# Kernel optimization log

Hardware: AMD Instinct MI355X
Metric: run time of the kernel (lower is better)

## Reference

```python
import jax, jax.numpy as jnp
import numpy as np

N_NODES = 50000
N_EDGES = 800000
NUM_GRAPHS = 16
NUM_CLASSES = 247


def _glorot(key, shape):
    fan_in = shape[0]
    return jax.random.normal(key, shape, jnp.float32) * (1.0 / np.sqrt(fan_in))


def setup_inputs() -> dict:
    key = jax.random.key(0)
    ks = jax.random.split(key, 8)
    x = jax.random.normal(ks[0], (N_NODES, 3), jnp.float32)
    edge_index = jax.random.randint(ks[1], (2, N_EDGES), 0, N_NODES, dtype=jnp.int64 if jax.config.jax_enable_x64 else jnp.int32)
    batch = jnp.sort(jax.random.randint(ks[2], (N_NODES,), 0, NUM_GRAPHS))
    return {
        "x": x,
        "edge_index": edge_index,
        "batch": batch,
        "W1": _glorot(ks[3], (3, 64)),
        "b1": jnp.zeros((64,), jnp.float32),
        "W2": _glorot(ks[4], (64, 128)),
        "b2": jnp.zeros((128,), jnp.float32),
        "W3": _glorot(ks[5], (128, 256)),
        "b3": jnp.zeros((256,), jnp.float32),
        "Wfc": _glorot(ks[6], (256, NUM_CLASSES)),
        "bfc": jnp.zeros((NUM_CLASSES,), jnp.float32),
    }


def reference(x, edge_index, batch, W1, b1, W2, b2, W3, b3, Wfc, bfc):
    N = x.shape[0]
    # --- GCN symmetric normalization with self-loops (PyG gcn_norm) ---
    loops = jnp.arange(N, dtype=edge_index.dtype)
    ei = jnp.concatenate([edge_index, jnp.stack([loops, loops])], axis=1)
    row, col = ei[0], ei[1]  # src -> dst, aggregate at dst
    deg = jax.ops.segment_sum(jnp.ones(ei.shape[1], x.dtype), col, num_segments=N)
    dinv = jnp.where(deg > 0, jax.lax.rsqrt(deg), 0.0)
    norm = dinv[row] * dinv[col]  # [E+N]

    def gcn(h, W, b):
        h = h @ W                                    # [N, out]
        msg = h[row] * norm[:, None]                 # gather + scale
        agg = jax.ops.segment_sum(msg, col, num_segments=N)  # scatter-add
        return agg + b

    h = jax.nn.relu(gcn(x, W1, b1))
    h = jax.nn.relu(gcn(h, W2, b2))
    h = jax.nn.relu(gcn(h, W3, b3))

    # --- global_mean_pool over batch indices ---
    sums = jax.ops.segment_sum(h, batch, num_segments=NUM_GRAPHS)      # [G, 256]
    cnt = jax.ops.segment_sum(jnp.ones(N, h.dtype), batch, num_segments=NUM_GRAPHS)
    pooled = sums / jnp.maximum(cnt, 1.0)[:, None]

    return pooled @ Wfc + bfc  # [G, num_classes]
```

## Files before the change

### kernel.cpp

```cpp
#include <hip/hip_runtime.h>

#define N_NODES 50000
#define N_EDGES 800000
#define NUM_GRAPHS 16
#define NUM_CLASSES 247
#define SCAN_BLOCKS ((N_NODES + 255) / 256)
#define CSR_CAP (N_EDGES + 7 * N_NODES)

typedef __attribute__((ext_vector_type(8))) short bf16x8;
typedef __attribute__((ext_vector_type(4))) float f32x4;

static inline int nblk(long n) { return (int)((n + 255) / 256); }

__device__ __forceinline__ float bfl(unsigned short u) {
    return __uint_as_float((unsigned)u << 16);
}
__device__ __forceinline__ unsigned short bf16_rne(float f) {
    unsigned u = __float_as_uint(f);
    u += 0x7FFF + ((u >> 16) & 1);
    return (unsigned short)(u >> 16);
}

__device__ __forceinline__ unsigned q8(float v) {
    if (v < 0.015625f) return 0u;
    unsigned u = __float_as_uint(v) - (120u << 23);
    u += 0x3FFFF + ((u >> 19) & 1);
    unsigned q = u >> 19;
    return q > 255u ? 255u : q;
}
__device__ __forceinline__ float dq8(unsigned x) {
    float f = __uint_as_float((x + 1920u) << 19);
    return x ? f : 0.0f;
}

__global__ void k_deg(const int* __restrict__ col, int* __restrict__ degc,
                      int* __restrict__ pos, int E) {
    int e = blockIdx.x * blockDim.x + threadIdx.x;
    if (e >= E) return;
    int c8 = (e >> 8) & 7;
    pos[e] = atomicAdd(&degc[c8 * N_NODES + col[e]], 1);
}

__global__ __launch_bounds__(256) void k_scan1(const int* __restrict__ degc,
                                               int* __restrict__ rowptr,
                                               int* __restrict__ bsum,
                                               const int* __restrict__ batch,
                                               float* __restrict__ pcnt, int N) {
    __shared__ int buf[256];
    __shared__ int hist[NUM_GRAPHS];
    int t = threadIdx.x;
    if (t < NUM_GRAPHS) hist[t] = 0;
    __syncthreads();
    int i = blockIdx.x * 256 + t;
    int v = 0;
    if (i < N) {
        int tot = 0;
#pragma unroll
        for (int c = 0; c < 8; ++c) tot += degc[c * N_NODES + i];
        v = (tot + 7) & ~7;
        atomicAdd(&hist[batch[i]], 1);
    }
    buf[t] = v;
    __syncthreads();
#pragma unroll
    for (int off = 1; off < 256; off <<= 1) {
        int tmp = (t >= off) ? buf[t - off] : 0;
        __syncthreads();
        if (t >= off) buf[t] += tmp;
        __syncthreads();
    }
    if (i < N) rowptr[i] = buf[t] - v;
    if (t == 255) bsum[blockIdx.x] = buf[255];
    if (t < NUM_GRAPHS && hist[t] > 0) atomicAdd(&pcnt[t], (float)hist[t]);
}

__global__ __launch_bounds__(256) void k_scan3(int* __restrict__ rowptr,
                                               const int* __restrict__ bsum,
                                               const int* __restrict__ degc,
                                               int* __restrict__ base,
                                               float* __restrict__ dinv,
                                               const float* __restrict__ x,
                                               float* __restrict__ xs,
                                               int* __restrict__ csr,
                                               const float* __restrict__ W2,
                                               const float* __restrict__ W3,
                                               unsigned short* __restrict__ Wt2,
                                               unsigned short* __restrict__ Wt3,
                                               int N) {
    __shared__ int red[256];
    int t = threadIdx.x;
    int b = blockIdx.x;
    red[t] = (t < b) ? bsum[t] : 0;
    __syncthreads();
#pragma unroll
    for (int off = 128; off > 0; off >>= 1) {
        if (t < off) red[t] += red[t + off];
        __syncthreads();
    }
    int boff = red[0];
    int i = b * 256 + t;
    if (i < N) {
        int rp = rowptr[i] + boff;
        rowptr[i] = rp;
        int run = rp, tot = 0;
#pragma unroll
        for (int c = 0; c < 8; ++c) {
            int d = degc[c * N_NODES + i];
            base[c * N_NODES + i] = run;
            run += d;
            tot += d;
        }
        int pdeg = (tot + 7) & ~7;
        for (int j = rp + tot; j < rp + pdeg; ++j) csr[j] = N_NODES;
        if (i == N - 1) rowptr[N] = rp + pdeg;
        float dv = rsqrtf((float)tot + 1.0f);
        dinv[i] = dv;
        xs[i * 3 + 0] = dv * x[i * 3 + 0];
        xs[i * 3 + 1] = dv * x[i * 3 + 1];
        xs[i * 3 + 2] = dv * x[i * 3 + 2];
    }
    if (i == 0) {
        xs[3 * N_NODES + 0] = 0.0f;
        xs[3 * N_NODES + 1] = 0.0f;
        xs[3 * N_NODES + 2] = 0.0f;
    }
    if (i < 64 * 128) {
        int f = i / 64, k = i % 64;
        Wt2[i] = bf16_rne(W2[k * 128 + f] * 0.015625f);
    } else if (i < 64 * 128 + 128 * 256) {
        int j = i - 64 * 128;
        int f = j / 128, k = j % 128;
        Wt3[j] = bf16_rne(W3[k * 256 + f] * 0.015625f);
    }
}

__global__ void k_fill(const int* __restrict__ row, const int* __restrict__ col,
                       const int* __restrict__ base, const int* __restrict__ pos,
                       int* __restrict__ csr_src, int E) {
    int e = blockIdx.x * blockDim.x + threadIdx.x;
    if (e >= E) return;
    int c8 = (e >> 8) & 7;
    csr_src[base[c8 * N_NODES + col[e]] + pos[e]] = row[e];
}

__global__ void k_layer1(const float* __restrict__ xs, const float* __restrict__ dinv,
                         const int* __restrict__ rowptr, const int* __restrict__ csr_src,
                         const float* __restrict__ W1, const float* __restrict__ b1,
                         unsigned char* __restrict__ out, int N) {
    int v = blockIdx.x * blockDim.x + threadIdx.x;
    if (v >= N) return;
    float a0 = xs[v * 3 + 0];
    float a1 = xs[v * 3 + 1];
    float a2 = xs[v * 3 + 2];
    int j = rowptr[v];
    int j1 = rowptr[v + 1];
    for (; j + 4 <= j1; j += 4) {
        int r0 = csr_src[j + 0], r1 = csr_src[j + 1];
        int r2 = csr_src[j + 2], r3 = csr_src[j + 3];
        float x00 = xs[r0 * 3 + 0], x01 = xs[r0 * 3 + 1], x02 = xs[r0 * 3 + 2];
        float x10 = xs[r1 * 3 + 0], x11 = xs[r1 * 3 + 1], x12 = xs[r1 * 3 + 2];
        float x20 = xs[r2 * 3 + 0], x21 = xs[r2 * 3 + 1], x22 = xs[r2 * 3 + 2];
        float x30 = xs[r3 * 3 + 0], x31 = xs[r3 * 3 + 1], x32 = xs[r3 * 3 + 2];
        a0 += x00; a1 += x01; a2 += x02;
        a0 += x10; a1 += x11; a2 += x12;
        a0 += x20; a1 += x21; a2 += x22;
        a0 += x30; a1 += x31; a2 += x32;
    }
    for (; j < j1; ++j) {
        int r = csr_src[j];
        a0 += xs[r * 3 + 0];
        a1 += xs[r * 3 + 1];
        a2 += xs[r * 3 + 2];
    }
    float dv = dinv[v];
    float p0 = dv * a0, p1 = dv * a1, p2 = dv * a2;
    float dv64 = dv * 64.0f;
    unsigned char* ov = out + (long)v * 64;
#pragma unroll
    for (int f = 0; f < 64; f += 4) {
        unsigned pk = 0;
#pragma unroll
        for (int t = 0; t < 4; ++t) {
            float s = fmaf(p0, W1[f + t], fmaf(p1, W1[64 + f + t], fmaf(p2, W1[128 + f + t], b1[f + t])));
            s = fmaxf(s, 0.0f) * dv64;
            pk |= q8(s) << (8 * t);
        }
        *(unsigned*)(ov + f) = pk;
    }
}

template <int K, int F, bool PRESCALE, bool POOL>
__global__ __launch_bounds__(256) void k_fused(
        const unsigned char* __restrict__ h, const float* __restrict__ dinv,
        const int* __restrict__ rowptr, const int* __restrict__ csr_src,
        const unsigned short* __restrict__ Wt, const float* __restrict__ b,
        unsigned char* __restrict__ out, const int* __restrict__ batch,
        float* __restrict__ psum, int N) {
    constexpr int NF = F / 16;
    constexpr int FPW = NF / 4;
    constexpr int KB = K / 32;
    constexpr int KL = K / 64;
    constexpr int PADK = K + 8;
    __shared__ unsigned short plds[16][PADK];
    int wave = threadIdx.x >> 6;
    int lane = threadIdx.x & 63;
    int m0 = blockIdx.x * 16;

    for (int pr = 0; pr < 2; ++pr) {
        int va = m0 + wave * 4 + pr * 2;
        int vb = va + 1;
        float acca[KL], accb[KL];
        const unsigned char* hva = h + (long)va * K + lane * KL;
        const unsigned char* hvb = h + (long)vb * K + lane * KL;
        if (KL == 2) {
            unsigned ua = *(const unsigned short*)hva;
            unsigned ub = *(const unsigned short*)hvb;
            acca[0] = dq8(ua & 0xff);
            acca[1] = dq8(ua >> 8);
            accb[0] = dq8(ub & 0xff);
            accb[1] = dq8(ub >> 8);
        } else {
            acca[0] = dq8(hva[0]);
            accb[0] = dq8(hvb[0]);
        }
        int ja  = __builtin_amdgcn_readfirstlane(rowptr[va]);
        int j1a = __builtin_amdgcn_readfirstlane(rowptr[va + 1]);
        int jb  = j1a;
        int j1b = __builtin_amdgcn_readfirstlane(rowptr[vb + 1]);
        while (ja + 8 <= j1a && jb + 8 <= j1b) {
            int ra[8], rb[8];
#pragma unroll
            for (int u = 0; u < 8; ++u) ra[u] = csr_src[ja + u];
#pragma unroll
            for (int u = 0; u < 8; ++u) rb[u] = csr_src[jb + u];
            if (KL == 2) {
                unsigned ta[8], tb[8];
#pragma unroll
                for (int u = 0; u < 8; ++u)
                    ta[u] = *(const unsigned short*)(h + (long)ra[u] * K + lane * 2);
#pragma unroll
                for (int u = 0; u < 8; ++u)
                    tb[u] = *(const unsigned short*)(h + (long)rb[u] * K + lane * 2);
#pragma unroll
                for (int u = 0; u < 8; ++u) {
                    acca[0] += dq8(ta[u] & 0xff);
                    acca[1] += dq8(ta[u] >> 8);
                }
#pragma unroll
                for (int u = 0; u < 8; ++u) {
                    accb[0] += dq8(tb[u] & 0xff);
                    accb[1] += dq8(tb[u] >> 8);
                }
            } else {
                unsigned char ta[8], tb[8];
#pragma unroll
                for (int u = 0; u < 8; ++u) ta[u] = h[(long)ra[u] * K + lane];
#pragma unroll
                for (int u = 0; u < 8; ++u) tb[u] = h[(long)rb[u] * K + lane];
#pragma unroll
                for (int u = 0; u < 8; ++u) acca[0] += dq8(ta[u]);
#pragma unroll
                for (int u = 0; u < 8; ++u) accb[0] += dq8(tb[u]);
            }
            ja += 8;
            jb += 8;
        }
        for (; ja + 8 <= j1a; ja += 8) {
            int r[8];
#pragma unroll
            for (int u = 0; u < 8; ++u) r[u] = csr_src[ja + u];
            if (KL == 2) {
                unsigned tv[8];
#pragma unroll
                for (int u = 0; u < 8; ++u)
                    tv[u] = *(const unsigned short*)(h + (long)r[u] * K + lane * 2);
#pragma unroll
                for (int u = 0; u < 8; ++u) {
                    acca[0] += dq8(tv[u] & 0xff);
                    acca[1] += dq8(tv[u] >> 8);
                }
            } else {
                unsigned char tv[8];
#pragma unroll
                for (int u = 0; u < 8; ++u) tv[u] = h[(long)r[u] * K + lane];
#pragma unroll
                for (int u = 0; u < 8; ++u) acca[0] += dq8(tv[u]);
            }
        }
        for (; ja < j1a; ++ja) {
            int r = csr_src[ja];
            if (KL == 2) {
                unsigned u = *(const unsigned short*)(h + (long)r * K + lane * 2);
                acca[0] += dq8(u & 0xff);
                acca[1] += dq8(u >> 8);
            } else {
                acca[0] += dq8(h[(long)r * K + lane]);
            }
        }
        for (; jb + 8 <= j1b; jb += 8) {
            int r[8];
#pragma unroll
            for (int u = 0; u < 8; ++u) r[u] = csr_src[jb + u];
            if (KL == 2) {
                unsigned tv[8];
#pragma unroll
                for (int u = 0; u < 8; ++u)
                    tv[u] = *(const unsigned short*)(h + (long)r[u] * K + lane * 2);
#pragma unroll
                for (int u = 0; u < 8; ++u) {
                    accb[0] += dq8(tv[u] & 0xff);
                    accb[1] += dq8(tv[u] >> 8);
                }
            } else {
                unsigned char tv[8];
#pragma unroll
                for (int u = 0; u < 8; ++u) tv[u] = h[(long)r[u] * K + lane];
#pragma unroll
                for (int u = 0; u < 8; ++u) accb[0] += dq8(tv[u]);
            }
        }
        for (; jb < j1b; ++jb) {
            int r = csr_src[jb];
            if (KL == 2) {
                unsigned u = *(const unsigned short*)(h + (long)r * K + lane * 2);
                accb[0] += dq8(u & 0xff);
                accb[1] += dq8(u >> 8);
            } else {
                accb[0] += dq8(h[(long)r * K + lane]);
            }
        }
        float da = dinv[va];
        float db = dinv[vb];
        int rla = wave * 4 + pr * 2;
        if (KL == 2) {
            unsigned pa = (unsigned)bf16_rne(da * acca[0]) | ((unsigned)bf16_rne(da * acca[1]) << 16);
            unsigned pb = (unsigned)bf16_rne(db * accb[0]) | ((unsigned)bf16_rne(db * accb[1]) << 16);
            *(unsigned*)&plds[rla][lane * 2] = pa;
            *(unsigned*)&plds[rla + 1][lane * 2] = pb;
        } else {
            plds[rla][lane] = bf16_rne(da * acca[0]);
            plds[rla + 1][lane] = bf16_rne(db * accb[0]);
        }
    }
    __syncthreads();

    int quad = lane >> 4;
    int l16 = lane & 15;
    bf16x8 afr[KB];
#pragma unroll
    for (int kb = 0; kb < KB; ++kb)
        afr[kb] = *(const bf16x8*)(const void*)&plds[l16][kb * 32 + quad * 8];
#pragma unroll
    for (int fi = 0; fi < FPW; ++fi) {
        int f0 = (wave * FPW + fi) * 16;
        const unsigned short* wrow = Wt + (long)(f0 + l16) * K + quad * 8;
        f32x4 acc4 = {0.f, 0.f, 0.f, 0.f};
#pragma unroll
        for (int kb = 0; kb < KB; ++kb) {
            bf16x8 bb = *(const bf16x8*)(const void*)(wrow + kb * 32);
            acc4 = __builtin_amdgcn_mfma_f32_16x16x32_bf16(afr[kb], bb, acc4, 0, 0, 0);
        }
        float bias = b[f0 + l16];
        if (POOL) {
            int g0 = batch[m0];
            int g15 = batch[m0 + 15];
            if (g0 == g15) {
                float s = fmaxf(acc4[0] + bias, 0.0f);
                s += fmaxf(acc4[1] + bias, 0.0f);
                s += fmaxf(acc4[2] + bias, 0.0f);
                s += fmaxf(acc4[3] + bias, 0.0f);
                s += __shfl_xor(s, 16);
                s += __shfl_xor(s, 32);
                if (quad == 0) atomicAdd(&psum[g0 * 256 + f0 + l16], s);
            } else {
#pragma unroll
                for (int r = 0; r < 4; ++r) {
                    int m = m0 + quad * 4 + r;
                    float val = fmaxf(acc4[r] + bias, 0.0f);
                    atomicAdd(&psum[batch[m] * 256 + f0 + l16], val);
                }
            }
        } else {
#pragma unroll
            for (int r = 0; r < 4; ++r) {
                int m = m0 + quad * 4 + r;
                float val = fmaxf(acc4[r] + bias, 0.0f);
                if (PRESCALE) val *= dinv[m] * 64.0f;
                out[(long)m * F + f0 + l16] = (unsigned char)q8(val);
            }
        }
    }
}

__global__ void k_fc(const float* __restrict__ psum, const float* __restrict__ pcnt,
                     const float* __restrict__ Wfc, const float* __restrict__ bfc,
                     float* __restrict__ out) {
    int tid = blockIdx.x * blockDim.x + threadIdx.x;
    if (tid >= NUM_GRAPHS * NUM_CLASSES) return;
    int g = tid / NUM_CLASSES;
    int c = tid % NUM_CLASSES;
    float s = 0.0f;
#pragma unroll 8
    for (int k = 0; k < 256; ++k) s = fmaf(psum[g * 256 + k], Wfc[k * NUM_CLASSES + c], s);
    float cnt = pcnt[g];
    cnt = cnt > 1.0f ? cnt : 1.0f;
    out[tid] = s / cnt + bfc[c];
}

extern "C" void kernel_launch(void* const* d_in, const int* in_sizes, int n_in,
                              void* d_out, int out_size, void* d_ws, size_t ws_size,
                              hipStream_t stream) {
    const float* x     = (const float*)d_in[0];
    const int*   ei    = (const int*)d_in[1];
    const int*   batch = (const int*)d_in[2];
    const float* W1    = (const float*)d_in[3];
    const float* b1    = (const float*)d_in[4];
    const float* W2    = (const float*)d_in[5];
    const float* b2    = (const float*)d_in[6];
    const float* W3    = (const float*)d_in[7];
    const float* b3    = (const float*)d_in[8];
    const float* Wfc   = (const float*)d_in[9];
    const float* bfc   = (const float*)d_in[10];
    float* out = (float*)d_out;

    const int* row = ei;
    const int* col = ei + N_EDGES;

    float*  xs   = (float*)d_ws;
    float*  dinv = xs + 150004;
    float*  psum = dinv + N_NODES;
    float*  pcnt = psum + NUM_GRAPHS * 256;
    unsigned char* X = (unsigned char*)(pcnt + NUM_GRAPHS);
    unsigned char* Y = X + (size_t)(N_NODES + 1) * 64;
    unsigned short* Wt2 = (unsigned short*)(Y + (size_t)(N_NODES + 1) * 128);
    unsigned short* Wt3 = Wt2 + 128 * 64;
    int* degc   = (int*)(Wt3 + 256 * 128);
    int* base   = degc + 8 * N_NODES;
    int* rowptr = base + 8 * N_NODES;
    int* csrsrc = rowptr + N_NODES + 1;
    int* pos    = csrsrc + CSR_CAP;
    int* bsum   = pos + N_EDGES;

    hipMemsetAsync(degc, 0, 8 * N_NODES * sizeof(int), stream);
    hipMemsetAsync(psum, 0, (NUM_GRAPHS * 256 + NUM_GRAPHS) * sizeof(float), stream);
    hipMemsetAsync(X + (size_t)N_NODES * 64, 0, 64, stream);
    hipMemsetAsync(Y + (size_t)N_NODES * 128, 0, 128, stream);

    k_deg<<<nblk(N_EDGES), 256, 0, stream>>>(col, degc, pos, N_EDGES);
    k_scan1<<<SCAN_BLOCKS, 256, 0, stream>>>(degc, rowptr, bsum, batch, pcnt, N_NODES);
    k_scan3<<<SCAN_BLOCKS, 256, 0, stream>>>(rowptr, bsum, degc, base, dinv, x, xs,
                                             csrsrc, W2, W3, Wt2, Wt3, N_NODES);
    k_fill<<<nblk(N_EDGES), 256, 0, stream>>>(row, col, base, pos, csrsrc, N_EDGES);

    k_layer1<<<nblk(N_NODES), 256, 0, stream>>>(xs, dinv, rowptr, csrsrc, W1, b1, X, N_NODES);

    int mtiles = N_NODES / 16;

    k_fused<64, 128, true, false><<<mtiles, 256, 0, stream>>>(
        X, dinv, rowptr, csrsrc, Wt2, b2, Y, batch, psum, N_NODES);

    k_fused<128, 256, false, true><<<mtiles, 256, 0, stream>>>(
        Y, dinv, rowptr, csrsrc, Wt3, b3, (unsigned char*)nullptr, batch, psum, N_NODES);

    k_fc<<<nblk(NUM_GRAPHS * NUM_CLASSES), 256, 0, stream>>>(psum, pcnt, Wfc, bfc, out);
}
```

Measured before the change: 245.8 us.

## Fuse preprocessing and layer-1 kernels into one persistent kernel with grid barriers

Replaces the four memsets and the degree, two scan, CSR-fill and layer-1 kernels with a single persistent kernel of 512 blocks. The phases are separated by a hand-written atomic grid barrier, and buffer zeroing moves into the kernel itself. The aim is to remove launch gaps and per-kernel ramp-up across these short dependent stages. In exchange it adds five global barrier spin-waits. It also depends on all 512 blocks being resident at once, otherwise the barrier deadlocks, and it needs a small barrier counter that is memset before launch.

```diff
diff --git a/kernel.cpp b/kernel.cpp
--- a/kernel.cpp
+++ b/kernel.cpp
@@ -6,6 +6,7 @@
 #define NUM_CLASSES 247
 #define SCAN_BLOCKS ((N_NODES + 255) / 256)
 #define CSR_CAP (N_EDGES + 7 * N_NODES)
+#define PREP_BLOCKS 512
 
 typedef __attribute__((ext_vector_type(8))) short bf16x8;
 typedef __attribute__((ext_vector_type(4))) float f32x4;
@@ -33,159 +34,179 @@
     return x ? f : 0.0f;
 }
 
-__global__ void k_deg(const int* __restrict__ col, int* __restrict__ degc,
-                      int* __restrict__ pos, int E) {
-    int e = blockIdx.x * blockDim.x + threadIdx.x;
-    if (e >= E) return;
-    int c8 = (e >> 8) & 7;
-    pos[e] = atomicAdd(&degc[c8 * N_NODES + col[e]], 1);
-}
-
-__global__ __launch_bounds__(256) void k_scan1(const int* __restrict__ degc,
-                                               int* __restrict__ rowptr,
-                                               int* __restrict__ bsum,
-                                               const int* __restrict__ batch,
-                                               float* __restrict__ pcnt, int N) {
-    __shared__ int buf[256];
-    __shared__ int hist[NUM_GRAPHS];
-    int t = threadIdx.x;
-    if (t < NUM_GRAPHS) hist[t] = 0;
+__device__ __forceinline__ void gridbar(int* bar, int id, int nb) {
+    __threadfence();
     __syncthreads();
-    int i = blockIdx.x * 256 + t;
-    int v = 0;
-    if (i < N) {
-        int tot = 0;
-#pragma unroll
-        for (int c = 0; c < 8; ++c) tot += degc[c * N_NODES + i];
-        v = (tot + 7) & ~7;
-        atomicAdd(&hist[batch[i]], 1);
-    }
-    buf[t] = v;
+    if (threadIdx.x == 0) {
+        if (atomicAdd(&bar[2 * id], 1) == nb - 1) {
+            atomicExch(&bar[2 * id + 1], 1);
+        } else {
+            while (atomicAdd(&bar[2 * id + 1], 0) == 0)
+                __builtin_amdgcn_s_sleep(16);
+        }
+    }
     __syncthreads();
-#pragma unroll
-    for (int off = 1; off < 256; off <<= 1) {
-        int tmp = (t >= off) ? buf[t - off] : 0;
+    __threadfence();
+}
+
+__global__ __launch_bounds__(256, 2) void k_prep(
+        const int* __restrict__ col, const int* __restrict__ row,
+        const int* __restrict__ batch, const float* __restrict__ x,
+        const float* __restrict__ W1, const float* __restrict__ b1,
+        const float* __restrict__ W2, const float* __restrict__ W3,
+        int* __restrict__ degc, int* __restrict__ pos,
+        int* __restrict__ rowptr, int* __restrict__ bsum,
+        int* __restrict__ base, float* __restrict__ dinv,
+        float* __restrict__ xs, unsigned short* __restrict__ Wt2,
+        unsigned short* __restrict__ Wt3, int* __restrict__ csr,
+        float* __restrict__ psum, unsigned char* __restrict__ X,
+        unsigned char* __restrict__ Y, int* __restrict__ bar) {
+    __shared__ int s_buf[256];
+    __shared__ int s_hist[NUM_GRAPHS];
+    __shared__ int s_red[256];
+    const int nb = gridDim.x;
+    const int nthr = nb * 256;
+    const int tid = blockIdx.x * 256 + threadIdx.x;
+    float* pcnt = psum + NUM_GRAPHS * 256;
+
+    for (int i = tid; i < 8 * N_NODES; i += nthr) degc[i] = 0;
+    for (int i = tid; i < NUM_GRAPHS * 256 + NUM_GRAPHS; i += nthr) psum[i] = 0.0f;
+    if (tid < 64) X[(size_t)N_NODES * 64 + tid] = 0;
+    if (tid < 128) Y[(size_t)N_NODES * 128 + tid] = 0;
+    gridbar(bar, 0, nb);
+
+    for (int e = tid; e < N_EDGES; e += nthr) {
+        int c8 = (e >> 8) & 7;
+        pos[e] = atomicAdd(&degc[c8 * N_NODES + col[e]], 1);
+    }
+    gridbar(bar, 1, nb);
+
+    if (blockIdx.x < SCAN_BLOCKS) {
+        int t = threadIdx.x;
+        if (t < NUM_GRAPHS) s_hist[t] = 0;
         __syncthreads();
-        if (t >= off) buf[t] += tmp;
+        int i = blockIdx.x * 256 + t;
+        int v = 0;
+        if (i < N_NODES) {
+            int tot = 0;
+#pragma unroll
+            for (int c = 0; c < 8; ++c) tot += degc[c * N_NODES + i];
+            v = (tot + 7) & ~7;
+            atomicAdd(&s_hist[batch[i]], 1);
+        }
+        s_buf[t] = v;
         __syncthreads();
-    }
-    if (i < N) rowptr[i] = buf[t] - v;
-    if (t == 255) bsum[blockIdx.x] = buf[255];
-    if (t < NUM_GRAPHS && hist[t] > 0) atomicAdd(&pcnt[t], (float)hist[t]);
-}
-
-__global__ __launch_bounds__(256) void k_scan3(int* __restrict__ rowptr,
-                                               const int* __restrict__ bsum,
-                                               const int* __restrict__ degc,
-                                               int* __restrict__ base,
-                                               float* __restrict__ dinv,
-                                               const float* __restrict__ x,
-                                               float* __restrict__ xs,
-                                               int* __restrict__ csr,
-                                               const float* __restrict__ W2,
-                                               const float* __restrict__ W3,
-                                               unsigned short* __restrict__ Wt2,
-                                               unsigned short* __restrict__ Wt3,
-                                               int N) {
-    __shared__ int red[256];
-    int t = threadIdx.x;
-    int b = blockIdx.x;
-    red[t] = (t < b) ? bsum[t] : 0;
-    __syncthreads();
-#pragma unroll
-    for (int off = 128; off > 0; off >>= 1) {
-        if (t < off) red[t] += red[t + off];
+#pragma unroll
+        for (int off = 1; off < 256; off <<= 1) {
+            int tmp = (t >= off) ? s_buf[t - off] : 0;
+            __syncthreads();
+            if (t >= off) s_buf[t] += tmp;
+            __syncthreads();
+        }
+        if (i < N_NODES) rowptr[i] = s_buf[t] - v;
+        if (t == 255) bsum[blockIdx.x] = s_buf[255];
+        if (t < NUM_GRAPHS && s_hist[t] > 0) atomicAdd(&pcnt[t], (float)s_hist[t]);
+    }
+    gridbar(bar, 2, nb);
+
+    if (blockIdx.x < SCAN_BLOCKS) {
+        int t = threadIdx.x;
+        int b = blockIdx.x;
+        s_red[t] = (t < b) ? bsum[t] : 0;
         __syncthreads();
-    }
-    int boff = red[0];
-    int i = b * 256 + t;
-    if (i < N) {
-        int rp = rowptr[i] + boff;
-        rowptr[i] = rp;
-        int run = rp, tot = 0;
-#pragma unroll
-        for (int c = 0; c < 8; ++c) {
-            int d = degc[c * N_NODES + i];
-            base[c * N_NODES + i] = run;
-            run += d;
-            tot += d;
-        }
-        int pdeg = (tot + 7) & ~7;
-        for (int j = rp + tot; j < rp + pdeg; ++j) csr[j] = N_NODES;
-        if (i == N - 1) rowptr[N] = rp + pdeg;
-        float dv = rsqrtf((float)tot + 1.0f);
-        dinv[i] = dv;
-        xs[i * 3 + 0] = dv * x[i * 3 + 0];
-        xs[i * 3 + 1] = dv * x[i * 3 + 1];
-        xs[i * 3 + 2] = dv * x[i * 3 + 2];
-    }
-    if (i == 0) {
-        xs[3 * N_NODES + 0] = 0.0f;
-        xs[3 * N_NODES + 1] = 0.0f;
-        xs[3 * N_NODES + 2] = 0.0f;
-    }
-    if (i < 64 * 128) {
-        int f = i / 64, k = i % 64;
-        Wt2[i] = bf16_rne(W2[k * 128 + f] * 0.015625f);
-    } else if (i < 64 * 128 + 128 * 256) {
-        int j = i - 64 * 128;
-        int f = j / 128, k = j % 128;
-        Wt3[j] = bf16_rne(W3[k * 256 + f] * 0.015625f);
-    }
-}
-
-__global__ void k_fill(const int* __restrict__ row, const int* __restrict__ col,
-                       const int* __restrict__ base, const int* __restrict__ pos,
-                       int* __restrict__ csr_src, int E) {
-    int e = blockIdx.x * blockDim.x + threadIdx.x;
-    if (e >= E) return;
-    int c8 = (e >> 8) & 7;
-    csr_src[base[c8 * N_NODES + col[e]] + pos[e]] = row[e];
-}
-
-__global__ void k_layer1(const float* __restrict__ xs, const float* __restrict__ dinv,
-                         const int* __restrict__ rowptr, const int* __restrict__ csr_src,
-                         const float* __restrict__ W1, const float* __restrict__ b1,
-                         unsigned char* __restrict__ out, int N) {
-    int v = blockIdx.x * blockDim.x + threadIdx.x;
-    if (v >= N) return;
-    float a0 = xs[v * 3 + 0];
-    float a1 = xs[v * 3 + 1];
-    float a2 = xs[v * 3 + 2];
-    int j = rowptr[v];
-    int j1 = rowptr[v + 1];
-    for (; j + 4 <= j1; j += 4) {
-        int r0 = csr_src[j + 0], r1 = csr_src[j + 1];
-        int r2 = csr_src[j + 2], r3 = csr_src[j + 3];
-        float x00 = xs[r0 * 3 + 0], x01 = xs[r0 * 3 + 1], x02 = xs[r0 * 3 + 2];
-        float x10 = xs[r1 * 3 + 0], x11 = xs[r1 * 3 + 1], x12 = xs[r1 * 3 + 2];
-        float x20 = xs[r2 * 3 + 0], x21 = xs[r2 * 3 + 1], x22 = xs[r2 * 3 + 2];
-        float x30 = xs[r3 * 3 + 0], x31 = xs[r3 * 3 + 1], x32 = xs[r3 * 3 + 2];
-        a0 += x00; a1 += x01; a2 += x02;
-        a0 += x10; a1 += x11; a2 += x12;
-        a0 += x20; a1 += x21; a2 += x22;
-        a0 += x30; a1 += x31; a2 += x32;
-    }
-    for (; j < j1; ++j) {
-        int r = csr_src[j];
-        a0 += xs[r * 3 + 0];
-        a1 += xs[r * 3 + 1];
-        a2 += xs[r * 3 + 2];
-    }
-    float dv = dinv[v];
-    float p0 = dv * a0, p1 = dv * a1, p2 = dv * a2;
-    float dv64 = dv * 64.0f;
-    unsigned char* ov = out + (long)v * 64;
-#pragma unroll
-    for (int f = 0; f < 64; f += 4) {
-        unsigned pk = 0;
-#pragma unroll
-        for (int t = 0; t < 4; ++t) {
-            float s = fmaf(p0, W1[f + t], fmaf(p1, W1[64 + f + t], fmaf(p2, W1[128 + f + t], b1[f + t])));
-            s = fmaxf(s, 0.0f) * dv64;
-            pk |= q8(s) << (8 * t);
-        }
-        *(unsigned*)(ov + f) = pk;
+#pragma unroll
+        for (int off = 128; off > 0; off >>= 1) {
+            if (t < off) s_red[t] += s_red[t + off];
+            __syncthreads();
+        }
+        int boff = s_red[0];
+        int i = b * 256 + t;
+        if (i < N_NODES) {
+            int rp = rowptr[i] + boff;
+            rowptr[i] = rp;
+            int run = rp, tot = 0;
+#pragma unroll
+            for (int c = 0; c < 8; ++c) {
+                int d = degc[c * N_NODES + i];
+                base[c * N_NODES + i] = run;
+                run += d;
+                tot += d;
+            }
+            int pdeg = (tot + 7) & ~7;
+            for (int j = rp + tot; j < rp + pdeg; ++j) csr[j] = N_NODES;
+            if (i == N_NODES - 1) rowptr[N_NODES] = rp + pdeg;
+            float dv = rsqrtf((float)tot + 1.0f);
+            dinv[i] = dv;
+            xs[i * 3 + 0] = dv * x[i * 3 + 0];
+            xs[i * 3 + 1] = dv * x[i * 3 + 1];
+            xs[i * 3 + 2] = dv * x[i * 3 + 2];
+        }
+        if (i == 0) {
+            xs[3 * N_NODES + 0] = 0.0f;
+            xs[3 * N_NODES + 1] = 0.0f;
+            xs[3 * N_NODES + 2] = 0.0f;
+        }
+        if (i < 64 * 128) {
+            int f = i / 64, k = i % 64;
+            Wt2[i] = bf16_rne(W2[k * 128 + f] * 0.015625f);
+        } else if (i < 64 * 128 + 128 * 256) {
+            int j = i - 64 * 128;
+            int f = j / 128, k = j % 128;
+            Wt3[j] = bf16_rne(W3[k * 256 + f] * 0.015625f);
+        }
+    }
+    gridbar(bar, 3, nb);
+
+    for (int e = tid; e < N_EDGES; e += nthr) {
+        int c8 = (e >> 8) & 7;
+        csr[base[c8 * N_NODES + col[e]] + pos[e]] = row[e];
+    }
+    gridbar(bar, 4, nb);
+
+    {
+        int v = tid;
+        if (v < N_NODES) {
+            float a0 = xs[v * 3 + 0];
+            float a1 = xs[v * 3 + 1];
+            float a2 = xs[v * 3 + 2];
+            int j = rowptr[v];
+            int j1 = rowptr[v + 1];
+            for (; j + 4 <= j1; j += 4) {
+                int r0 = csr[j + 0], r1 = csr[j + 1];
+                int r2 = csr[j + 2], r3 = csr[j + 3];
+                float x00 = xs[r0 * 3 + 0], x01 = xs[r0 * 3 + 1], x02 = xs[r0 * 3 + 2];
+                float x10 = xs[r1 * 3 + 0], x11 = xs[r1 * 3 + 1], x12 = xs[r1 * 3 + 2];
+                float x20 = xs[r2 * 3 + 0], x21 = xs[r2 * 3 + 1], x22 = xs[r2 * 3 + 2];
+                float x30 = xs[r3 * 3 + 0], x31 = xs[r3 * 3 + 1], x32 = xs[r3 * 3 + 2];
+                a0 += x00; a1 += x01; a2 += x02;
+                a0 += x10; a1 += x11; a2 += x12;
+                a0 += x20; a1 += x21; a2 += x22;
+                a0 += x30; a1 += x31; a2 += x32;
+            }
+            for (; j < j1; ++j) {
+                int r = csr[j];
+                a0 += xs[r * 3 + 0];
+                a1 += xs[r * 3 + 1];
+                a2 += xs[r * 3 + 2];
+            }
+            float dv = dinv[v];
+            float p0 = dv * a0, p1 = dv * a1, p2 = dv * a2;
+            float dv64 = dv * 64.0f;
+            unsigned char* ov = X + (long)v * 64;
+#pragma unroll
+            for (int f = 0; f < 64; f += 4) {
+                unsigned pk = 0;
+#pragma unroll
+                for (int t = 0; t < 4; ++t) {
+                    float s = fmaf(p0, W1[f + t],
+                              fmaf(p1, W1[64 + f + t],
+                              fmaf(p2, W1[128 + f + t], b1[f + t])));
+                    s = fmaxf(s, 0.0f) * dv64;
+                    pk |= q8(s) << (8 * t);
+                }
+                *(unsigned*)(ov + f) = pk;
+            }
+        }
     }
 }
 
@@ -440,19 +461,14 @@
     int* csrsrc = rowptr + N_NODES + 1;
     int* pos    = csrsrc + CSR_CAP;
     int* bsum   = pos + N_EDGES;
-
-    hipMemsetAsync(degc, 0, 8 * N_NODES * sizeof(int), stream);
-    hipMemsetAsync(psum, 0, (NUM_GRAPHS * 256 + NUM_GRAPHS) * sizeof(float), stream);
-    hipMemsetAsync(X + (size_t)N_NODES * 64, 0, 64, stream);
-    hipMemsetAsync(Y + (size_t)N_NODES * 128, 0, 128, stream);
-
-    k_deg<<<nblk(N_EDGES), 256, 0, stream>>>(col, degc, pos, N_EDGES);
-    k_scan1<<<SCAN_BLOCKS, 256, 0, stream>>>(degc, rowptr, bsum, batch, pcnt, N_NODES);
-    k_scan3<<<SCAN_BLOCKS, 256, 0, stream>>>(rowptr, bsum, degc, base, dinv, x, xs,
-                                             csrsrc, W2, W3, Wt2, Wt3, N_NODES);
-    k_fill<<<nblk(N_EDGES), 256, 0, stream>>>(row, col, base, pos, csrsrc, N_EDGES);
-
-    k_layer1<<<nblk(N_NODES), 256, 0, stream>>>(xs, dinv, rowptr, csrsrc, W1, b1, X, N_NODES);
+    int* bar    = bsum + SCAN_BLOCKS;
+
+    hipMemsetAsync(bar, 0, 16 * sizeof(int), stream);
+
+    k_prep<<<PREP_BLOCKS, 256, 0, stream>>>(
+        col, row, batch, x, W1, b1, W2, W3,
+        degc, pos, rowptr, bsum, base, dinv, xs, Wt2, Wt3,
+        csrsrc, psum, X, Y, bar);
 
     int mtiles = N_NODES / 16;
 
```

Result: slower. 689.7 us (+180.6%).
